# Optimization experiments

Measured on AMD Instinct MI355X. Metric: run time of the kernel, lower is better.

Reference implementation:

```python
import jax, jax.numpy as jnp
import numpy as np

N_QUBITS = 4
N_LAYERS = 3
N_FEATURES = 64
BATCH = 524288


def setup_inputs() -> dict:
    key = jax.random.key(0)
    k1, k2, k3, k4 = jax.random.split(key, 4)
    x = jax.random.normal(k1, (BATCH, N_FEATURES), jnp.float32)
    # nn.Linear(64, 4) params
    lim = 1.0 / np.sqrt(N_FEATURES)
    W_pre = jax.random.uniform(k2, (N_QUBITS, N_FEATURES), jnp.float32, -lim, lim)
    b_pre = jax.random.uniform(k3, (N_QUBITS,), jnp.float32, -lim, lim)
    # quantum circuit weights: randn * 0.1
    qweights = jax.random.normal(k4, (N_LAYERS, N_QUBITS, 2), jnp.float32) * 0.1
    return {"x": x, "W_pre": W_pre, "b_pre": b_pre, "qweights": qweights}


def _coef(theta, n):
    # reshape scalar or [B] angle to broadcast against [B, 2,..,2] (n-1 trailing dims after slicing)
    return jnp.reshape(theta, (-1,) + (1,) * (n - 1))


def _apply_ry(state, wire, theta):
    # RY(t) = [[cos t/2, -sin t/2], [sin t/2, cos t/2]] applied on `wire`
    n = state.ndim - 1
    s = jnp.moveaxis(state, 1 + wire, -1)
    a, b = s[..., 0], s[..., 1]
    c = _coef(jnp.cos(theta / 2), n)
    sn = _coef(jnp.sin(theta / 2), n)
    out = jnp.stack([c * a - sn * b, sn * a + c * b], axis=-1)
    return jnp.moveaxis(out, -1, 1 + wire)


def _apply_rz(state, wire, theta):
    # RZ(t) = diag(e^{-i t/2}, e^{+i t/2})
    n = state.ndim - 1
    s = jnp.moveaxis(state, 1 + wire, -1)
    half = _coef(theta / 2, n)
    out = jnp.stack([jnp.exp(-1j * half) * s[..., 0],
                     jnp.exp(1j * half) * s[..., 1]], axis=-1)
    return jnp.moveaxis(out, -1, 1 + wire)


def _apply_cnot(state, ctrl, tgt):
    s = jnp.moveaxis(state, (1 + ctrl, 1 + tgt), (-2, -1))
    s = jnp.concatenate([s[..., 0:1, :], s[..., 1:2, ::-1]], axis=-2)
    return jnp.moveaxis(s, (-2, -1), (1 + ctrl, 1 + tgt))


def _circuit(angles, qweights):
    # batched 4-qubit statevector simulation; state shape [B, 2,2,2,2] (wire 0 = MSB)
    B, n = angles.shape
    nl = qweights.shape[0]
    state = jnp.zeros((B,) + (2,) * n, jnp.complex64)
    state = state.at[(slice(None),) + (0,) * n].set(1.0)
    for w in range(n):
        state = _apply_ry(state, w, angles[:, w])
    for l in range(nl):
        for w in range(n):
            state = _apply_ry(state, w, qweights[l, w, 0])
            state = _apply_rz(state, w, qweights[l, w, 1])
        for w in range(n):
            state = _apply_cnot(state, w, (w + 1) % n)
    probs = state.real ** 2 + state.imag ** 2  # [B, 2,2,2,2] float32
    exps = []
    for w in range(n):
        marg = jnp.moveaxis(probs, 1 + w, 1).reshape(B, 2, -1).sum(-1)  # [B, 2]
        exps.append(marg[:, 0] - marg[:, 1])  # <Z_w>
    return jnp.stack(exps, axis=1)  # [B, n]


def reference(x, W_pre, b_pre, qweights):
    angles = jnp.tanh(x @ W_pre.T + b_pre)  # [B, n_qubits]
    return _circuit(angles, qweights).astype(jnp.float32)
```

## Files before the change

kernel.cpp:

```cpp
#include <hip/hip_runtime.h>
#include <hip/hip_bf16.h>
#include <cmath>


typedef __attribute__((ext_vector_type(8))) short bf16x8;
typedef __attribute__((ext_vector_type(4))) float f32x4;

__global__ __launch_bounds__(256) void qprep_kernel(
    const float* __restrict__ qw,
    float* __restrict__ A_out)
{
  __shared__ float sre[16][17];
  __shared__ float sim[16][17];
  __shared__ float M[4][16][16];
  const int tid = threadIdx.x;
  const int col = tid >> 4;
  const int u   = tid & 15;

  sre[col][u] = (u == col) ? 1.0f : 0.0f;
  sim[col][u] = 0.0f;
  __syncthreads();

#pragma unroll
  for (int l = 0; l < 3; ++l) {
#pragma unroll
    for (int w = 0; w < 4; ++w) {
      const int mask = 8 >> w;
      float sh, ch, sh2, ch2;
      __sincosf(0.5f * qw[(l * 4 + w) * 2 + 0], &sh, &ch);
      __sincosf(0.5f * qw[(l * 4 + w) * 2 + 1], &sh2, &ch2);
      const int ua = u & ~mask, ub = u | mask;
      const float ar = sre[col][ua], ai = sim[col][ua];
      const float br = sre[col][ub], bi = sim[col][ub];
      __syncthreads();
      float nr, ni;
      if (u & mask) { nr = sh * ar + ch * br; ni = sh * ai + ch * bi; }
      else          { nr = ch * ar - sh * br; ni = ch * ai - sh * bi; }
      float rr, ri;
      if (u & mask) { rr = ch2 * nr - sh2 * ni; ri = ch2 * ni + sh2 * nr; }
      else          { rr = ch2 * nr + sh2 * ni; ri = ch2 * ni - sh2 * nr; }
      sre[col][u] = rr; sim[col][u] = ri;
      __syncthreads();
    }
    int src = u;
    if (src & 1) src ^= 8;
    if (src & 2) src ^= 1;
    if (src & 4) src ^= 2;
    if (src & 8) src ^= 4;
    const float pr = sre[col][src], pi = sim[col][src];
    __syncthreads();
    sre[col][u] = pr; sim[col][u] = pi;
    __syncthreads();
  }

  for (int idx = tid; idx < 1024; idx += 256) {
    const int w = idx >> 8, s = (idx >> 4) & 15, t = idx & 15;
    const int mask = 8 >> w;
    float acc = 0.0f;
#pragma unroll
    for (int uu = 0; uu < 16; ++uu) {
      const float z = (uu & mask) ? -1.0f : 1.0f;
      acc += z * (sre[s][uu] * sre[t][uu] + sim[s][uu] * sim[t][uu]);
    }
    M[w][s][t] = acc;
  }
  __syncthreads();

  for (int idx = tid; idx < 324; idx += 256) {
    const int w = idx & 3, pq = idx >> 2;
    const int p = pq / 9, q = pq % 9;
    const int i0 = p / 3, i1 = p % 3, i2 = q / 3, i3 = q % 3;
    float acc = 0.0f;
#pragma unroll
    for (int comb = 0; comb < 16; ++comb) {
      int s = 0, t = 0;
      float coef = 0.0625f;
      int j;
      j = (comb >> 3) & 1; s |= j << 3; t |= ((i0 == 2) ? (j ^ 1) : j) << 3; if (i0 == 1 && j) coef = -coef;
      j = (comb >> 2) & 1; s |= j << 2; t |= ((i1 == 2) ? (j ^ 1) : j) << 2; if (i1 == 1 && j) coef = -coef;
      j = (comb >> 1) & 1; s |= j << 1; t |= ((i2 == 2) ? (j ^ 1) : j) << 1; if (i2 == 1 && j) coef = -coef;
      j = comb & 1;        s |= j;      t |= ((i3 == 2) ? (j ^ 1) : j);      if (i3 == 1 && j) coef = -coef;
      acc = fmaf(coef, M[w][s][t], acc);
    }
    A_out[idx] = acc;
  }
}

__device__ __forceinline__ bf16x8 pack8(const float4 va, const float4 vb) {
  union { bf16x8 v; __hip_bfloat16 h[8]; } u;
  u.h[0] = __float2bfloat16(va.x); u.h[1] = __float2bfloat16(va.y);
  u.h[2] = __float2bfloat16(va.z); u.h[3] = __float2bfloat16(va.w);
  u.h[4] = __float2bfloat16(vb.x); u.h[5] = __float2bfloat16(vb.y);
  u.h[6] = __float2bfloat16(vb.z); u.h[7] = __float2bfloat16(vb.w);
  return u.v;
}

__device__ __forceinline__ float ftanh(float a) {
  return 1.0f - 2.0f * __builtin_amdgcn_rcpf(__expf(2.0f * a) + 1.0f);
}

#define LDSUB(V0, V1, V2, V3, R0, S) {                                      \
  const float* rp_ = x + ((R0) + (size_t)((S) * 16 + arow)) * 64 + kgrp * 8;\
  V0 = *reinterpret_cast<const float4*>(rp_);                               \
  V1 = *reinterpret_cast<const float4*>(rp_ + 4);                           \
  V2 = *reinterpret_cast<const float4*>(rp_ + 32);                          \
  V3 = *reinterpret_cast<const float4*>(rp_ + 36); }

#define DOMFMA(V0, V1, V2, V3, M, LB) {                                     \
  const bf16x8 af0_ = pack8(V0, V1);                                        \
  const bf16x8 af1_ = pack8(V2, V3);                                        \
  f32x4 acc_ = __builtin_amdgcn_mfma_f32_16x16x32_bf16(af0_, wf0, zero, 0, 0, 0); \
  acc_ = __builtin_amdgcn_mfma_f32_16x16x32_bf16(af1_, wf1, acc_, 0, 0, 0); \
  if (arow < 4) {                                                           \
    _Pragma("unroll")                                                       \
    for (int r_ = 0; r_ < 4; ++r_)                                          \
      myld[(LB) * 256 + ((M) * 16 + kgrp * 4 + r_) * 4 + arow] = acc_[r_];  \
  } }

#define TAIL(R0, LB) {                                                      \
  asm volatile("s_waitcnt lgkmcnt(0)" ::: "memory");                        \
  __builtin_amdgcn_sched_barrier(0);                                        \
  const float4 ang =                                                        \
      *reinterpret_cast<const float4*>(&myld[(LB) * 256 + lane * 4]);       \
  const float t0 = ftanh(ang.x + bp[0]);                                    \
  const float t1 = ftanh(ang.y + bp[1]);                                    \
  const float t2 = ftanh(ang.z + bp[2]);                                    \
  const float t3 = ftanh(ang.w + bp[3]);                                    \
  float c0, s0, c1, s1, c2, s2, c3, s3;                                     \
  __sincosf(t0, &s0, &c0); __sincosf(t1, &s1, &c1);                         \
  __sincosf(t2, &s2, &c2); __sincosf(t3, &s3, &c3);                         \
  const float g[9] = {1.f, c1, s1, c0, c0 * c1, c0 * s1,                    \
                      s0, s0 * c1, s0 * s1};                                \
  const float h[9] = {1.f, c3, s3, c2, c2 * c3, c2 * s3,                    \
                      s2, s2 * c3, s2 * s3};                                \
  float e0 = 0.f, e1 = 0.f, e2 = 0.f, e3 = 0.f;                             \
  _Pragma("unroll")                                                         \
  for (int p_ = 0; p_ < 9; ++p_) {                                          \
    _Pragma("unroll")                                                       \
    for (int q_ = 0; q_ < 9; ++q_) {                                        \
      const float4 a4 = Aws[p_ * 9 + q_];                                   \
      const float tt = g[p_] * h[q_];                                       \
      e0 = fmaf(a4.x, tt, e0); e1 = fmaf(a4.y, tt, e1);                     \
      e2 = fmaf(a4.z, tt, e2); e3 = fmaf(a4.w, tt, e3);                     \
    }                                                                       \
  }                                                                         \
  reinterpret_cast<float4*>(out)[(R0) + lane] =                             \
      make_float4(e0, e1, e2, e3);                                          \
  asm volatile("" ::: "memory"); }

__global__ __launch_bounds__(256)
__attribute__((amdgpu_waves_per_eu(4, 4)))
void qmain_kernel(
    const float* __restrict__ x,
    const float* __restrict__ Wp,
    const float* __restrict__ bp,
    const float4* __restrict__ Aws,
    float* __restrict__ out)
{
  __shared__ alignas(16) float wlds[4][2][256];

  const int tid  = threadIdx.x;
  const int lane = tid & 63;
  const int wid  = tid >> 6;
  const int arow = lane & 15;
  const int kgrp = lane >> 4;
  float* myld = &wlds[wid][0][0];

  const size_t wrow0 = ((size_t)blockIdx.x * 4 + wid) * 128;

  bf16x8 wf0, wf1;
#pragma unroll
  for (int j = 0; j < 8; ++j) {
    if (arow < 4) {
      union { short s; __hip_bfloat16 h; } u0, u1;
      u0.h = __float2bfloat16(Wp[arow * 64 + 0  + kgrp * 8 + j]);
      u1.h = __float2bfloat16(Wp[arow * 64 + 32 + kgrp * 8 + j]);
      wf0[j] = u0.s; wf1[j] = u1.s;
    } else {
      wf0[j] = 0; wf1[j] = 0;
    }
  }
  const f32x4 zero = {0.f, 0.f, 0.f, 0.f};

  const size_t r0 = wrow0;
  const size_t r1 = wrow0 + 64;

  float4 a0, a1, a2, a3, b0, b1, b2, b3;

  LDSUB(a0, a1, a2, a3, r0, 0);
  LDSUB(b0, b1, b2, b3, r0, 1);
  DOMFMA(a0, a1, a2, a3, 0, 0); LDSUB(a0, a1, a2, a3, r0, 2);
  DOMFMA(b0, b1, b2, b3, 1, 0); LDSUB(b0, b1, b2, b3, r0, 3);
  DOMFMA(a0, a1, a2, a3, 2, 0); LDSUB(a0, a1, a2, a3, r1, 0);
  DOMFMA(b0, b1, b2, b3, 3, 0); LDSUB(b0, b1, b2, b3, r1, 1);

  TAIL(r0, 0);

  DOMFMA(a0, a1, a2, a3, 0, 1); LDSUB(a0, a1, a2, a3, r1, 2);
  DOMFMA(b0, b1, b2, b3, 1, 1); LDSUB(b0, b1, b2, b3, r1, 3);
  DOMFMA(a0, a1, a2, a3, 2, 1);
  DOMFMA(b0, b1, b2, b3, 3, 1);

  TAIL(r1, 1);
}

extern "C" void kernel_launch(void* const* d_in, const int* in_sizes, int n_in,
                              void* d_out, int out_size, void* d_ws, size_t ws_size,
                              hipStream_t stream) {
  const float* x  = (const float*)d_in[0];
  const float* Wp = (const float*)d_in[1];
  const float* bp = (const float*)d_in[2];
  const float* qw = (const float*)d_in[3];
  float* out = (float*)d_out;
  float* A = (float*)d_ws;
  (void)n_in; (void)out_size; (void)ws_size;

  qprep_kernel<<<1, 256, 0, stream>>>(qw, A);

  const int B = in_sizes[0] / 64;
  qmain_kernel<<<B / 512, 256, 0, stream>>>(x, Wp, bp,
                                            (const float4*)A, out);
}
```

Measured before the change: 36.27 us.

## Stage x tiles through swizzled per-wave LDS with coalesced global loads

Each lane used to load row-strided float4 pieces of x straight into registers. Now each wave issues fully lane-contiguous float4 global loads, writes them into a double-buffered per-wave LDS area using an XOR swizzle, and reads them back in the MFMA A-fragment layout. The loads are software-pipelined three subtiles deep so global latency overlaps with the MFMA and tail work. The goal is better coalescing of the dominant HBM stream. The cost is extra LDS writes and reads plus more LDS per block, which may limit occupancy.

```diff
diff --git a/kernel.cpp b/kernel.cpp
--- a/kernel.cpp
+++ b/kernel.cpp
@@ -99,29 +99,37 @@
   return 1.0f - 2.0f * __builtin_amdgcn_rcpf(__expf(2.0f * a) + 1.0f);
 }
 
-#define LDSUB(V0, V1, V2, V3, R0, S) {                                      \
-  const float* rp_ = x + ((R0) + (size_t)((S) * 16 + arow)) * 64 + kgrp * 8;\
-  V0 = *reinterpret_cast<const float4*>(rp_);                               \
-  V1 = *reinterpret_cast<const float4*>(rp_ + 4);                           \
-  V2 = *reinterpret_cast<const float4*>(rp_ + 32);                          \
-  V3 = *reinterpret_cast<const float4*>(rp_ + 36); }
-
-#define DOMFMA(V0, V1, V2, V3, M, LB) {                                     \
-  const bf16x8 af0_ = pack8(V0, V1);                                        \
-  const bf16x8 af1_ = pack8(V2, V3);                                        \
+#define ISSUE(S, R0, R1, R2, R3) {                                          \
+  const float4* g_ = xs4 + (wrow0 + (size_t)((S) * 16)) * 16 + lane;        \
+  R0 = g_[0]; R1 = g_[64]; R2 = g_[128]; R3 = g_[192]; }
+
+#define WRITE(R0, R1, R2, R3, S) {                                          \
+  float* d_ = sb + ((S) & 1) * 1024;                                        \
+  *reinterpret_cast<float4*>(d_ + wsA)        = R0;                         \
+  *reinterpret_cast<float4*>(d_ + wsB + 256)  = R1;                         \
+  *reinterpret_cast<float4*>(d_ + wsA + 512)  = R2;                         \
+  *reinterpret_cast<float4*>(d_ + wsB + 768)  = R3; }
+
+#define CONSUME(S) {                                                        \
+  const float* s_ = sb + ((S) & 1) * 1024;                                  \
+  const float4 f0 = *reinterpret_cast<const float4*>(s_ + ((cb_ + 0) ^ rw_)); \
+  const float4 f1 = *reinterpret_cast<const float4*>(s_ + ((cb_ + 4) ^ rw_)); \
+  const float4 f2 = *reinterpret_cast<const float4*>(s_ + ((cb_ + 32) ^ rw_)); \
+  const float4 f3 = *reinterpret_cast<const float4*>(s_ + ((cb_ + 36) ^ rw_)); \
+  const bf16x8 af0_ = pack8(f0, f1);                                        \
+  const bf16x8 af1_ = pack8(f2, f3);                                        \
   f32x4 acc_ = __builtin_amdgcn_mfma_f32_16x16x32_bf16(af0_, wf0, zero, 0, 0, 0); \
   acc_ = __builtin_amdgcn_mfma_f32_16x16x32_bf16(af1_, wf1, acc_, 0, 0, 0); \
   if (arow < 4) {                                                           \
     _Pragma("unroll")                                                       \
     for (int r_ = 0; r_ < 4; ++r_)                                          \
-      myld[(LB) * 256 + ((M) * 16 + kgrp * 4 + r_) * 4 + arow] = acc_[r_];  \
+      ap[((((S) & 3) * 16) + kgrp * 4 + r_) * 4 + arow] = acc_[r_];         \
   } }
 
-#define TAIL(R0, LB) {                                                      \
+#define TAIL(R0) {                                                          \
   asm volatile("s_waitcnt lgkmcnt(0)" ::: "memory");                        \
   __builtin_amdgcn_sched_barrier(0);                                        \
-  const float4 ang =                                                        \
-      *reinterpret_cast<const float4*>(&myld[(LB) * 256 + lane * 4]);       \
+  const float4 ang = *reinterpret_cast<const float4*>(&ap[lane * 4]);       \
   const float t0 = ftanh(ang.x + bp[0]);                                    \
   const float t1 = ftanh(ang.y + bp[1]);                                    \
   const float t2 = ftanh(ang.z + bp[2]);                                    \
@@ -157,16 +165,23 @@
     const float4* __restrict__ Aws,
     float* __restrict__ out)
 {
-  __shared__ alignas(16) float wlds[4][2][256];
+  __shared__ alignas(16) float lds[4 * 2304];
 
   const int tid  = threadIdx.x;
   const int lane = tid & 63;
   const int wid  = tid >> 6;
   const int arow = lane & 15;
   const int kgrp = lane >> 4;
-  float* myld = &wlds[wid][0][0];
+  float* sb = &lds[wid * 2304];
+  float* ap = sb + 2048;
 
   const size_t wrow0 = ((size_t)blockIdx.x * 4 + wid) * 128;
+  const float4* xs4 = reinterpret_cast<const float4*>(x);
+
+  const int wsA = (lane * 4) ^ ((lane >> 4) << 2);
+  const int wsB = (lane * 4) ^ (((lane >> 4) + 4) << 2);
+  const int rw_ = (arow & 7) << 2;
+  const int cb_ = arow * 64 + kgrp * 8;
 
   bf16x8 wf0, wf1;
 #pragma unroll
@@ -185,23 +200,26 @@
   const size_t r0 = wrow0;
   const size_t r1 = wrow0 + 64;
 
-  float4 a0, a1, a2, a3, b0, b1, b2, b3;
-
-  LDSUB(a0, a1, a2, a3, r0, 0);
-  LDSUB(b0, b1, b2, b3, r0, 1);
-  DOMFMA(a0, a1, a2, a3, 0, 0); LDSUB(a0, a1, a2, a3, r0, 2);
-  DOMFMA(b0, b1, b2, b3, 1, 0); LDSUB(b0, b1, b2, b3, r0, 3);
-  DOMFMA(a0, a1, a2, a3, 2, 0); LDSUB(a0, a1, a2, a3, r1, 0);
-  DOMFMA(b0, b1, b2, b3, 3, 0); LDSUB(b0, b1, b2, b3, r1, 1);
-
-  TAIL(r0, 0);
-
-  DOMFMA(a0, a1, a2, a3, 0, 1); LDSUB(a0, a1, a2, a3, r1, 2);
-  DOMFMA(b0, b1, b2, b3, 1, 1); LDSUB(b0, b1, b2, b3, r1, 3);
-  DOMFMA(a0, a1, a2, a3, 2, 1);
-  DOMFMA(b0, b1, b2, b3, 3, 1);
-
-  TAIL(r1, 1);
+  float4 A0, A1, A2, A3, B0, B1, B2, B3, C0, C1, C2, C3;
+
+  ISSUE(0, A0, A1, A2, A3);
+  ISSUE(1, B0, B1, B2, B3);
+  ISSUE(2, C0, C1, C2, C3);
+  WRITE(A0, A1, A2, A3, 0);
+  WRITE(B0, B1, B2, B3, 1);
+  CONSUME(0); ISSUE(3, A0, A1, A2, A3); WRITE(C0, C1, C2, C3, 2);
+  CONSUME(1); ISSUE(4, B0, B1, B2, B3); WRITE(A0, A1, A2, A3, 3);
+  CONSUME(2); ISSUE(5, C0, C1, C2, C3); WRITE(B0, B1, B2, B3, 4);
+  CONSUME(3); ISSUE(6, A0, A1, A2, A3); WRITE(C0, C1, C2, C3, 5);
+
+  TAIL(r0);
+
+  CONSUME(4); ISSUE(7, B0, B1, B2, B3); WRITE(A0, A1, A2, A3, 6);
+  CONSUME(5); WRITE(B0, B1, B2, B3, 7);
+  CONSUME(6);
+  CONSUME(7);
+
+  TAIL(r1);
 }
 
 extern "C" void kernel_launch(void* const* d_in, const int* in_sizes, int n_in,
```

New measurement: 34.96 us, median of 2. 3.6% less time.
